# Performance work log

Measured on AMD Instinct MI355X. Metric: run time of the kernel, lower is better.

The kernel has to match this reference:

```python
import jax, jax.numpy as jnp
import numpy as np

TOP_K = 2

def setup_inputs() -> dict:
    key = jax.random.key(0)
    k1, k2, k3, k4 = jax.random.split(key, 4)
    B, S, D, E = 4, 4096, 2048, 8
    x = jax.random.normal(k1, (B, S, D), dtype=jnp.float32)
    w_g = jax.random.normal(k2, (E, D), dtype=jnp.float32) * (1.0 / np.sqrt(D))
    w_noise = jax.random.normal(k3, (E, D), dtype=jnp.float32) * (1.0 / np.sqrt(D))
    eps = jax.random.normal(k4, (B, S, E), dtype=jnp.float32)
    return {"x": x, "w_g": w_g, "w_noise": w_noise, "eps": eps}

def reference(x, w_g, w_noise, eps):
    # gate logits: [B, S, E]
    logits = jnp.einsum('bsd,ed->bse', x, w_g)
    # noisy top-k: logits += softplus(x @ w_noise.T) * eps
    noise = jax.nn.softplus(jnp.einsum('bsd,ed->bse', x, w_noise)) * eps
    logits = logits + noise
    top_k_logits, top_k_indices = jax.lax.top_k(logits, TOP_K)
    return (top_k_logits, top_k_indices)
```

## Files before the change

### kernel.cpp

```cpp
#include <hip/hip_runtime.h>
#include <math.h>

#define TOKENS 16384
#define DIM 2048
#define NE 8
#define NROWS 16
#define BLOCK 1024
#define WAVES_PER_BLOCK 16
#define GRID 256
#define TR 4
#define NGROUPS (TOKENS / TR)

__launch_bounds__(BLOCK, 4)
__global__ void router_kernel(const float* __restrict__ x,
                              const float* __restrict__ w_g,
                              const float* __restrict__ w_noise,
                              const float* __restrict__ eps,
                              float* __restrict__ out)
{
    __shared__ float wlds[NROWS * DIM];

    const int tid = threadIdx.x;

    {
        const float4* g4 = (const float4*)w_g;
        const float4* n4 = (const float4*)w_noise;
        float4* l4 = (float4*)wlds;
        #pragma unroll
        for (int i = tid; i < (NE * DIM) / 4; i += BLOCK) {
            l4[i] = g4[i];
            l4[i + (NE * DIM) / 4] = n4[i];
        }
    }

    const int lane = tid & 63;
    const int wave = blockIdx.x * WAVES_PER_BLOCK + (tid >> 6);
    const int t0 = wave * TR;

    float my_eps = 0.f;
    if (lane < 32) my_eps = eps[t0 * NE + lane];

    __syncthreads();

    const float4* x4  = (const float4*)x;
    const float4* wl4 = (const float4*)wlds;

    float V[64];
    #pragma unroll
    for (int v = 0; v < 64; ++v) V[v] = 0.f;

    float4 xv[TR];
    #pragma unroll
    for (int t = 0; t < TR; ++t)
        xv[t] = x4[(t0 + t) * (DIM / 4) + lane];

    #pragma unroll
    for (int k = 0; k < DIM / 256; ++k) {
        float4 xn[TR];
        if (k < DIM / 256 - 1) {
            #pragma unroll
            for (int t = 0; t < TR; ++t)
                xn[t] = x4[(t0 + t) * (DIM / 4) + (k + 1) * 64 + lane];
        }
        #pragma unroll
        for (int r = 0; r < NROWS; ++r) {
            const float4 w = wl4[r * (DIM / 4) + k * 64 + lane];
            #pragma unroll
            for (int t = 0; t < TR; ++t) {
                float a = V[r * 4 + t];
                a = fmaf(xv[t].x, w.x, a);
                a = fmaf(xv[t].y, w.y, a);
                a = fmaf(xv[t].z, w.z, a);
                a = fmaf(xv[t].w, w.w, a);
                V[r * 4 + t] = a;
            }
        }
        if (k < DIM / 256 - 1) {
            #pragma unroll
            for (int t = 0; t < TR; ++t) xv[t] = xn[t];
        }
    }

    #pragma unroll
    for (int s = 0; s < 6; ++s) {
        const int m = 1 << s;
        const int n = 64 >> s;
        #pragma unroll
        for (int j = 0; j < n / 2; ++j) {
            const float A = V[2 * j];
            const float B = V[2 * j + 1];
            const float As = __shfl_xor(A, m, 64);
            const float Bs = __shfl_xor(B, m, 64);
            V[j] = (lane & m) ? (B + Bs) : (A + As);
        }
    }
    const float mine = V[0];

    const float other = __shfl_xor(mine, 32, 64);

    if (lane < 32) {
        const int e = lane >> 2;
        const int t = lane & 3;
        const int tok = t0 + t;

        const float ev = __shfl(my_eps, (t << 3) | e, 64);

        const float nv = other;
        const float sp = fmaxf(nv, 0.f) + log1pf(expf(-fabsf(nv)));
        const float logit = fmaf(sp, ev, mine);

        float v1 = logit, v2 = -INFINITY;
        int   i1 = e,     i2 = 7;
        #pragma unroll
        for (int sm = 2; sm <= 4; ++sm) {
            const int m = 1 << sm;
            const float ov1 = __shfl_xor(v1, m, 64);
            const float ov2 = __shfl_xor(v2, m, 64);
            const int   oi1 = __shfl_xor(i1, m, 64);
            const int   oi2 = __shfl_xor(i2, m, 64);
            const bool firstA = (v1 > ov1) || (v1 == ov1 && i1 < oi1);
            const float nv1 = firstA ? v1  : ov1;
            const int   ni1 = firstA ? i1  : oi1;
            const float ca  = firstA ? ov1 : v1;
            const int   cia = firstA ? oi1 : i1;
            const float cb  = firstA ? v2  : ov2;
            const int   cib = firstA ? i2  : oi2;
            const bool secondA = (ca > cb) || (ca == cb && cia < cib);
            v1 = nv1; i1 = ni1;
            v2 = secondA ? ca : cb;
            i2 = secondA ? cia : cib;
        }

        if (e == 0) {
            out[2 * tok]     = v1;
            out[2 * tok + 1] = v2;
            out[2 * TOKENS + 2 * tok]     = (float)i1;
            out[2 * TOKENS + 2 * tok + 1] = (float)i2;
        }
    }
}

extern "C" void kernel_launch(void* const* d_in, const int* in_sizes, int n_in,
                              void* d_out, int out_size, void* d_ws, size_t ws_size,
                              hipStream_t stream) {
    const float* x       = (const float*)d_in[0];
    const float* w_g     = (const float*)d_in[1];
    const float* w_noise = (const float*)d_in[2];
    const float* eps     = (const float*)d_in[3];
    float* out = (float*)d_out;

    router_kernel<<<GRID, BLOCK, 0, stream>>>(x, w_g, w_noise, eps, out);
}
```

Before: 33.76 us.

## Stream gate weights into double-buffered LDS chunks with async global_load_lds

Instead of loading all 16x2048 weights into LDS before any compute, each block stages quarter-chunks of w_g/w_noise into a double-buffered LDS region with global_load_lds and overlaps that staging with the FMA work on the previous chunk. Block size is halved and grid doubled, and odd and even waves process chunk halves in swapped order, presumably to spread LDS bank access. The first two reduction stages use DPP moves instead of shuffles, and the outputs are written as float2. The smaller LDS footprint may allow more resident blocks, at the cost of more barriers per block.

```diff
diff --git a/kernel.cpp b/kernel.cpp
--- a/kernel.cpp
+++ b/kernel.cpp
@@ -4,12 +4,60 @@
 #define TOKENS 16384
 #define DIM 2048
 #define NE 8
-#define NROWS 16
-#define BLOCK 1024
-#define WAVES_PER_BLOCK 16
-#define GRID 256
-#define TR 4
-#define NGROUPS (TOKENS / TR)
+#define BLOCK 512
+#define GRID 512
+
+template <int CTRL>
+__device__ __forceinline__ float dpp_mov(float v) {
+    return __int_as_float(__builtin_amdgcn_update_dpp(
+        0, __float_as_int(v), CTRL, 0xf, 0xf, true));
+}
+#define DPP_XOR1 0xB1
+#define DPP_XOR2 0x4E
+
+__device__ __forceinline__ void stage16(const float* g, float* l) {
+    __builtin_amdgcn_global_load_lds(
+        (const __attribute__((address_space(1))) void*)g,
+        (__attribute__((address_space(3))) void*)l, 16, 0, 0);
+}
+
+#define FMA_BODY(XBUF, K)                                                     \
+    {                                                                         \
+        const int kk = (K);                                                   \
+        const int fb = ((kk >> 1) & 1) * 2048 + (kk & 1) * 64;                \
+        _Pragma("unroll")                                                     \
+        for (int r = 0; r < 16; ++r) {                                        \
+            const float4 w = wl4[fb + r * 128 + lane];                        \
+            _Pragma("unroll")                                                 \
+            for (int t = 0; t < 4; ++t) {                                     \
+                float a = V[r * 4 + t];                                       \
+                a = fmaf(XBUF[t].x, w.x, a);                                  \
+                a = fmaf(XBUF[t].y, w.y, a);                                  \
+                a = fmaf(XBUF[t].z, w.z, a);                                  \
+                a = fmaf(XBUF[t].w, w.w, a);                                  \
+                V[r * 4 + t] = a;                                             \
+            }                                                                 \
+        }                                                                     \
+    }
+#define REFILL(XBUF, K)                                                       \
+    {                                                                         \
+        const int kk = (K);                                                   \
+        _Pragma("unroll")                                                     \
+        for (int t = 0; t < 4; ++t)                                           \
+            XBUF[t] = x4[(t0 + t) * (DIM / 4) + kk * 64 + lane];              \
+    }
+#define STAGE_Q(Q)                                                            \
+    {                                                                         \
+        const int q = (Q);                                                    \
+        float* dst = wlds + (q & 1) * 8192;                                   \
+        _Pragma("unroll")                                                     \
+        for (int i = 0; i < 2; ++i) {                                         \
+            stage16(w_g + wv * DIM + q * 512 + i * 256 + lane * 4,            \
+                    dst + wv * 512 + i * 256);                                \
+            stage16(w_noise + wv * DIM + q * 512 + i * 256 + lane * 4,        \
+                    dst + (wv + 8) * 512 + i * 256);                          \
+        }                                                                     \
+    }
 
 __launch_bounds__(BLOCK, 4)
 __global__ void router_kernel(const float* __restrict__ x,
@@ -18,77 +66,70 @@
                               const float* __restrict__ eps,
                               float* __restrict__ out)
 {
-    __shared__ float wlds[NROWS * DIM];
+    __shared__ float wlds[2 * 16 * 512];
 
-    const int tid = threadIdx.x;
+    const int tid  = threadIdx.x;
+    const int lane = tid & 63;
+    const int wv   = tid >> 6;
+    const int t0   = (blockIdx.x * 8 + wv) * 4;
+    const int off  = wv & 1;
 
-    {
-        const float4* g4 = (const float4*)w_g;
-        const float4* n4 = (const float4*)w_noise;
-        float4* l4 = (float4*)wlds;
-        #pragma unroll
-        for (int i = tid; i < (NE * DIM) / 4; i += BLOCK) {
-            l4[i] = g4[i];
-            l4[i + (NE * DIM) / 4] = n4[i];
-        }
-    }
+    const float4* x4  = (const float4*)x;
+    const float4* wl4 = (const float4*)wlds;
 
-    const int lane = tid & 63;
-    const int wave = blockIdx.x * WAVES_PER_BLOCK + (tid >> 6);
-    const int t0 = wave * TR;
+    STAGE_Q(0);
+    float4 xvA[4], xvB[4];
+    REFILL(xvA, off);
+    REFILL(xvB, 1 - off);
 
     float my_eps = 0.f;
     if (lane < 32) my_eps = eps[t0 * NE + lane];
-
-    __syncthreads();
-
-    const float4* x4  = (const float4*)x;
-    const float4* wl4 = (const float4*)wlds;
 
     float V[64];
     #pragma unroll
     for (int v = 0; v < 64; ++v) V[v] = 0.f;
 
-    float4 xv[TR];
-    #pragma unroll
-    for (int t = 0; t < TR; ++t)
-        xv[t] = x4[(t0 + t) * (DIM / 4) + lane];
+    __syncthreads();
+
+    STAGE_Q(1);
+    FMA_BODY(xvA, off);          REFILL(xvA, 2 + off);
+    FMA_BODY(xvB, 1 - off);      REFILL(xvB, 3 - off);
+    __syncthreads();
+
+    STAGE_Q(2);
+    FMA_BODY(xvA, 2 + off);      REFILL(xvA, 4 + off);
+    FMA_BODY(xvB, 3 - off);      REFILL(xvB, 5 - off);
+    __syncthreads();
+
+    STAGE_Q(3);
+    FMA_BODY(xvA, 4 + off);      REFILL(xvA, 6 + off);
+    FMA_BODY(xvB, 5 - off);      REFILL(xvB, 7 - off);
+    __syncthreads();
+
+    FMA_BODY(xvA, 6 + off);
+    FMA_BODY(xvB, 7 - off);
 
     #pragma unroll
-    for (int k = 0; k < DIM / 256; ++k) {
-        float4 xn[TR];
-        if (k < DIM / 256 - 1) {
-            #pragma unroll
-            for (int t = 0; t < TR; ++t)
-                xn[t] = x4[(t0 + t) * (DIM / 4) + (k + 1) * 64 + lane];
-        }
-        #pragma unroll
-        for (int r = 0; r < NROWS; ++r) {
-            const float4 w = wl4[r * (DIM / 4) + k * 64 + lane];
-            #pragma unroll
-            for (int t = 0; t < TR; ++t) {
-                float a = V[r * 4 + t];
-                a = fmaf(xv[t].x, w.x, a);
-                a = fmaf(xv[t].y, w.y, a);
-                a = fmaf(xv[t].z, w.z, a);
-                a = fmaf(xv[t].w, w.w, a);
-                V[r * 4 + t] = a;
-            }
-        }
-        if (k < DIM / 256 - 1) {
-            #pragma unroll
-            for (int t = 0; t < TR; ++t) xv[t] = xn[t];
-        }
+    for (int j = 0; j < 32; ++j) {
+        const float A = V[2 * j], B = V[2 * j + 1];
+        const float As = dpp_mov<DPP_XOR1>(A);
+        const float Bs = dpp_mov<DPP_XOR1>(B);
+        V[j] = (lane & 1) ? (B + Bs) : (A + As);
     }
-
     #pragma unroll
-    for (int s = 0; s < 6; ++s) {
+    for (int j = 0; j < 16; ++j) {
+        const float A = V[2 * j], B = V[2 * j + 1];
+        const float As = dpp_mov<DPP_XOR2>(A);
+        const float Bs = dpp_mov<DPP_XOR2>(B);
+        V[j] = (lane & 2) ? (B + Bs) : (A + As);
+    }
+    #pragma unroll
+    for (int s = 2; s < 6; ++s) {
         const int m = 1 << s;
         const int n = 64 >> s;
         #pragma unroll
         for (int j = 0; j < n / 2; ++j) {
-            const float A = V[2 * j];
-            const float B = V[2 * j + 1];
+            const float A = V[2 * j], B = V[2 * j + 1];
             const float As = __shfl_xor(A, m, 64);
             const float Bs = __shfl_xor(B, m, 64);
             V[j] = (lane & m) ? (B + Bs) : (A + As);
@@ -132,10 +173,8 @@
         }
 
         if (e == 0) {
-            out[2 * tok]     = v1;
-            out[2 * tok + 1] = v2;
-            out[2 * TOKENS + 2 * tok]     = (float)i1;
-            out[2 * TOKENS + 2 * tok + 1] = (float)i2;
+            *(float2*)&out[2 * tok] = make_float2(v1, v2);
+            *(float2*)&out[2 * TOKENS + 2 * tok] = make_float2((float)i1, (float)i2);
         }
     }
 }
```

New measurement: 45.75 us. 35.5% more time.
